# Optimization experiments

Measured on AMD Instinct MI355X. Metric: run time of the kernel, lower is better.

Reference implementation:

```python
import jax, jax.numpy as jnp
import numpy as np

K = 5            # kernel_size per pseudo-dim
N = 51200        # nodes
E = 819200       # edges (avg degree 16)
B = 64           # graphs in batch

# 2^dim corner offsets for degree-1 (linear) open B-spline in dim=2
_BITS = jnp.array([[0, 0], [0, 1], [1, 0], [1, 1]], dtype=jnp.int32)  # [4,2]

def spline_basis(pseudo):
    # pseudo: [E,2] in [0,1]. Returns basis [E,4], weight indices [E,4].
    v = pseudo * (K - 1)
    lo = jnp.clip(jnp.floor(v).astype(jnp.int32), 0, K - 2)   # [E,2]
    frac = v - lo.astype(pseudo.dtype)                        # [E,2]
    idx = lo[:, None, :] + _BITS[None]                        # [E,4,2]
    w = jnp.where(_BITS[None] == 1, frac[:, None, :], 1.0 - frac[:, None, :])
    basis = w.prod(-1)                                        # [E,4]
    widx = idx[..., 0] * K + idx[..., 1]                      # [E,4] in [0,25)
    return basis, widx

def spline_conv(x, src, dst, basis, widx, W, root, bias):
    # x:[N,Fin], W:[25,Fin,Fout], root:[Fin,Fout], bias:[Fout]
    n = x.shape[0]
    Z = jnp.einsum('ni,kio->nko', x, W)          # [N,25,Fout] per-node per-kernel transforms
    Zg = Z[src[:, None], widx]                   # [E,4,Fout] irregular gather
    msg = jnp.einsum('es,eso->eo', basis, Zg)    # [E,Fout]
    agg = jax.ops.segment_sum(msg, dst, num_segments=n)
    deg = jax.ops.segment_sum(jnp.ones_like(msg[:, 0]), dst, num_segments=n)
    agg = agg / jnp.maximum(deg, 1.0)[:, None]   # mean aggregation
    return agg + x @ root + bias

def setup_inputs():
    key = jax.random.key(0)
    ks = jax.random.split(key, 12)
    x = jax.random.normal(ks[0], (N, 7), jnp.float32)
    edge_index = jax.random.randint(ks[1], (2, E), 0, N, dtype=jnp.int32)
    pseudo = jax.random.uniform(ks[2], (E, 2), jnp.float32)
    slices = jnp.arange(B + 1, dtype=jnp.int32) * (N // B)   # graph boundaries
    W1 = jax.random.normal(ks[3], (K * K, 7, 32), jnp.float32) * 0.2
    root1 = jax.random.normal(ks[4], (7, 32), jnp.float32) * 0.2
    b1 = jnp.zeros((32,), jnp.float32)
    W2 = jax.random.normal(ks[5], (K * K, 32, 64), jnp.float32) * 0.1
    root2 = jax.random.normal(ks[6], (32, 64), jnp.float32) * 0.1
    b2 = jnp.zeros((64,), jnp.float32)
    fc_w = jax.random.normal(ks[7], (64, 30), jnp.float32) * 0.1
    fc_b = jnp.zeros((30,), jnp.float32)
    return {"x": x, "edge_index": edge_index, "pseudo": pseudo, "slices": slices,
            "W1": W1, "root1": root1, "b1": b1, "W2": W2, "root2": root2,
            "b2": b2, "fc_w": fc_w, "fc_b": fc_b}

def reference(x, edge_index, pseudo, slices, W1, root1, b1, W2, root2, b2, fc_w, fc_b):
    src, dst = edge_index[0], edge_index[1]
    basis, widx = spline_basis(pseudo)
    h = jax.nn.elu(spline_conv(x, src, dst, basis, widx, W1, root1, b1))
    h = jax.nn.elu(spline_conv(h, src, dst, basis, widx, W2, root2, b2))
    # batch_average: mean of node features per graph (slices = boundaries)
    gid = jnp.clip(jnp.searchsorted(slices, jnp.arange(N), side='right') - 1, 0, B - 1)
    sums = jax.ops.segment_sum(h, gid, num_segments=B)
    counts = (slices[1:] - slices[:-1]).astype(h.dtype)
    g = sums / jnp.maximum(counts, 1.0)[:, None]             # [B,64]
    # dropout is identity in eval mode
    logits = g @ fc_w + fc_b
    return jax.nn.log_softmax(logits, axis=-1)
```

## Files before the change

### kernel.cpp

```cpp
#include <hip/hip_runtime.h>
#include <hip/hip_fp16.h>
#include <math.h>

#define N_NODES 51200
#define N_EDGES 819200
#define NB 64
#define CAP 64

typedef _Float16 half8 __attribute__((ext_vector_type(8)));
typedef __attribute__((ext_vector_type(4))) float float4v;

__device__ __forceinline__ float eluf(float x) {
  return x > 0.f ? x : expm1f(x);
}

__device__ __forceinline__ void dec2(int w0, int w1, int c, float& basf, int& Kc) {
  int K = w0 >> 16;
  float f0 = __half2float(__ushort_as_half((unsigned short)(w1 & 0xFFFF)));
  float f1 = __half2float(__ushort_as_half((unsigned short)(((unsigned)w1) >> 16)));
  float b0 = (c & 2) ? f0 : 1.f - f0;
  float bv = (c & 1) ? f1 : 1.f - f1;
  Kc = K + (c >> 1) * 5 + (c & 1);
  basf = b0 * bv;
}

__device__ __forceinline__ void rmw16(unsigned* Tr, int Kc, int q, float bf, int4 hv) {
  __half2 bas = __float2half2_rn(bf);
  __half2* tp = (__half2*)&Tr[Kc * 16 + q * 4];
  const __half2* h = (const __half2*)&hv;
  __half2 t0 = tp[0], t1 = tp[1], t2 = tp[2], t3 = tp[3];
  tp[0] = __hfma2(bas, h[0], t0);
  tp[1] = __hfma2(bas, h[1], t1);
  tp[2] = __hfma2(bas, h[2], t2);
  tp[3] = __hfma2(bas, h[3], t3);
}

__global__ __launch_bounds__(256) void prep_scatter(
    const float* __restrict__ x, const float* __restrict__ W1,
    const float* __restrict__ root1, const float* __restrict__ W2,
    const float* __restrict__ root2, __half* __restrict__ xh,
    __half* __restrict__ W1T, __half* __restrict__ W2T,
    float* __restrict__ gbuf, const int* __restrict__ ei,
    const float* __restrict__ pseudo, int* __restrict__ cnt,
    int2* __restrict__ bucket) {
  int b = blockIdx.x, tid = threadIdx.x;
  if (b < 400) {
    int base = b * 2048 + tid;
#pragma unroll
    for (int u = 0; u < 8; u++) {
      int e = base + u * 256;
      int src = ei[e], dst = ei[N_EDGES + e];
      float v0 = pseudo[2 * e] * 4.f;
      float v1 = pseudo[2 * e + 1] * 4.f;
      int lo0 = min(max((int)floorf(v0), 0), 3);
      int lo1 = min(max((int)floorf(v1), 0), 3);
      float f0 = v0 - (float)lo0, f1 = v1 - (float)lo1;
      int K = lo0 * 5 + lo1;
      unsigned short u0 = __half_as_ushort(__float2half(f0));
      unsigned short u1 = __half_as_ushort(__float2half(f1));
      int w0 = src | (K << 16);
      int w1 = (int)((unsigned)u0 | ((unsigned)u1 << 16));
      int slot = atomicAdd(&cnt[dst], 1);
      if (slot < CAP) bucket[(size_t)dst * CAP + slot] = make_int2(w0, w1);
    }
    return;
  }
  int bb = b - 400;
  if (bb < 1600) {
    int idx = bb * 256 + tid;
    int n = idx >> 3, j = idx & 7;
    xh[idx] = __float2half((j < 7) ? x[n * 7 + j] : 0.f);
  } else if (bb < 1628) {
    int idx = (bb - 1600) * 256 + tid;
    int o = idx / 224, k = idx - o * 224;
    float v = 0.f;
    if (k < 200) {
      int cell = k >> 3, f = k & 7;
      if (f < 7) v = W1[(cell * 7 + f) * 32 + o];
    } else if (k < 207) {
      v = root1[(k - 200) * 32 + o];
    }
    W1T[idx] = __float2half(v);
  } else if (bb < 1836) {
    int idx = (bb - 1628) * 256 + tid;
    int o = idx / 832, k = idx - o * 832;
    float v = (k < 800) ? W2[k * 64 + o] : root2[(k - 800) * 64 + o];
    W2T[idx] = __float2half(v);
  } else {
    int idx = (bb - 1836) * 256 + tid;
    gbuf[idx] = 0.f;
  }
}

__global__ __launch_bounds__(256) void build_perm(const int* __restrict__ cnt,
                                                  int* __restrict__ perm) {
  __shared__ int hist[65];
  __shared__ int base_s[65];
  int g = blockIdx.x, tid = threadIdx.x;
  int n0 = g * 800;
  if (tid < 65) hist[tid] = 0;
  __syncthreads();
  for (int i = tid; i < 800; i += 256) {
    int d = min(cnt[n0 + i], 64);
    atomicAdd(&hist[d], 1);
  }
  __syncthreads();
  if (tid == 0) {
    int s = 0;
    for (int b = 0; b < 65; b++) { base_s[b] = s; s += hist[b]; }
  }
  __syncthreads();
  for (int i = tid; i < 800; i += 256) {
    int d = min(cnt[n0 + i], 64);
    int pos = atomicAdd(&base_s[d], 1);
    perm[n0 + pos] = n0 + i;
  }
}

#define L1N 16
__global__ __launch_bounds__(256) void fused_l1(const int2* __restrict__ bucket,
                                                const int* __restrict__ cnt,
                                                const int* __restrict__ perm,
                                                const unsigned* __restrict__ xh,
                                                const __half* __restrict__ W1T,
                                                const float* __restrict__ b1,
                                                unsigned short* __restrict__ h1h) {
  __shared__ unsigned T[L1N * 112];
  __shared__ float invdeg_s[L1N];
  __shared__ int pn_s[L1N];
  int tid = threadIdx.x;
  int n0 = blockIdx.x * L1N;
  for (int idx = tid; idx < 448; idx += 256)
    ((int4*)T)[idx] = make_int4(0, 0, 0, 0);
  if (tid < L1N) {
    int pn = perm[n0 + tid];
    pn_s[tid] = pn;
    invdeg_s[tid] = 1.f / fmaxf((float)cnt[pn], 1.f);
  }
  __syncthreads();
  if (tid < L1N * 4) {
    int row = tid >> 2, p = tid & 3;
    int n = pn_s[row];
    float dgc = fmaxf((float)cnt[n], 1.f);
    unsigned xv = xh[n * 4 + p];
    __half2 h = __hmul2(*(const __half2*)&xv, __float2half2_rn(dgc));
    T[row * 112 + 100 + p] = *(unsigned*)&h;
  }
  int wv = tid >> 6, l = tid & 63;
  int slot = l >> 4, c = (l >> 2) & 3, p = l & 3;
  int nn = wv * 4 + slot;
  int n = pn_s[nn];
  int dg = min(cnt[n], CAP);
  int dmax = dg;
  dmax = max(dmax, __shfl_xor(dmax, 16));
  dmax = max(dmax, __shfl_xor(dmax, 32));
  const int2* bk = bucket + (size_t)n * CAP;
  unsigned* Tr = &T[nn * 112];
  int4 ra0 = *(const int4*)(bk + 0);
  int4 rb0 = *(const int4*)(bk + 2);
  int4 ra1 = *(const int4*)(bk + 4);
  int4 rb1 = *(const int4*)(bk + 6);
  unsigned xv0 = xh[(ra0.x & 0xFFFF) * 4 + p];
  unsigned xv1 = xh[(ra0.z & 0xFFFF) * 4 + p];
  unsigned xv2 = xh[(rb0.x & 0xFFFF) * 4 + p];
  unsigned xv3 = xh[(rb0.z & 0xFFFF) * 4 + p];
  for (int j = 0; j < dmax; j += 4) {
    int jp = min(j + 8, CAP - 4);
    int4 ra2 = *(const int4*)(bk + jp);
    int4 rb2 = *(const int4*)(bk + jp + 2);
    unsigned nx0 = xh[(ra1.x & 0xFFFF) * 4 + p];
    unsigned nx1 = xh[(ra1.z & 0xFFFF) * 4 + p];
    unsigned nx2 = xh[(rb1.x & 0xFFFF) * 4 + p];
    unsigned nx3 = xh[(rb1.z & 0xFFFF) * 4 + p];
    bool a0 = j < dg, a1 = j + 1 < dg, a2 = j + 2 < dg, a3 = j + 3 < dg;
    float bf; int Kc;
    if (a0) { dec2(ra0.x, ra0.y, c, bf, Kc);
      __half2* tp = (__half2*)&Tr[Kc * 4 + p];
      *tp = __hfma2(__float2half2_rn(bf), *(const __half2*)&xv0, *tp); }
    if (a1) { dec2(ra0.z, ra0.w, c, bf, Kc);
      __half2* tp = (__half2*)&Tr[Kc * 4 + p];
      *tp = __hfma2(__float2half2_rn(bf), *(const __half2*)&xv1, *tp); }
    if (a2) { dec2(rb0.x, rb0.y, c, bf, Kc);
      __half2* tp = (__half2*)&Tr[Kc * 4 + p];
      *tp = __hfma2(__float2half2_rn(bf), *(const __half2*)&xv2, *tp); }
    if (a3) { dec2(rb0.z, rb0.w, c, bf, Kc);
      __half2* tp = (__half2*)&Tr[Kc * 4 + p];
      *tp = __hfma2(__float2half2_rn(bf), *(const __half2*)&xv3, *tp); }
    ra0 = ra1; rb0 = rb1; ra1 = ra2; rb1 = rb2;
    xv0 = nx0; xv1 = nx1; xv2 = nx2; xv3 = nx3;
  }
  __syncthreads();
  if (wv < 2) {
    int m = l & 15, quad = l >> 4;
    const char* abase = (const char*)T + m * 448 + quad * 16;
    const __half* bbase = W1T + (wv * 16 + m) * 224 + quad * 8;
    float4v acc = {0.f, 0.f, 0.f, 0.f};
#pragma unroll
    for (int it = 0; it < 7; it++) {
      half8 af = *(const half8*)(abase + it * 64);
      half8 bf = *(const half8*)(bbase + it * 32);
      acc = __builtin_amdgcn_mfma_f32_16x16x32_f16(af, bf, acc, 0, 0, 0);
    }
    int feat = wv * 16 + m;
    float bb = b1[feat];
#pragma unroll
    for (int r = 0; r < 4; r++) {
      int row = quad * 4 + r;
      float v = eluf(acc[r] * invdeg_s[row] + bb);
      h1h[(size_t)pn_s[row] * 32 + feat] = __half_as_ushort(__float2half(v));
    }
  }
}

#define L2N 16
__global__ __launch_bounds__(256) void fused_l2(const int2* __restrict__ bucket,
                                                const int* __restrict__ cnt,
                                                const int* __restrict__ perm,
                                                const unsigned* __restrict__ h1hu,
                                                const __half* __restrict__ W2T,
                                                const float* __restrict__ b2,
                                                float* __restrict__ gbuf) {
  __shared__ unsigned T16[L2N * 420];
  __shared__ float invdeg_s[L2N];
  __shared__ int pn_s[L2N];
  int tid = threadIdx.x;
  int n0 = blockIdx.x * L2N;
  for (int idx = tid; idx < 1680; idx += 256)
    ((int4*)T16)[idx] = make_int4(0, 0, 0, 0);
  if (tid < L2N) {
    int pn = perm[n0 + tid];
    pn_s[tid] = pn;
    invdeg_s[tid] = 1.f / fmaxf((float)cnt[pn], 1.f);
  }
  __syncthreads();
  {
    int row = tid >> 4, p = tid & 15;
    int n = pn_s[row];
    float dgc = fmaxf((float)cnt[n], 1.f);
    unsigned hv = h1hu[(size_t)n * 16 + p];
    __half2 h = __hmul2(*(const __half2*)&hv, __float2half2_rn(dgc));
    T16[row * 420 + 400 + p] = *(unsigned*)&h;
  }
  int wv = tid >> 6, l = tid & 63;
  int slot = l >> 4, c = (l >> 2) & 3, q = l & 3;
  int nn = wv * 4 + slot;
  int n = pn_s[nn];
  int dg = min(cnt[n], CAP);
  int dmax = dg;
  dmax = max(dmax, __shfl_xor(dmax, 16));
  dmax = max(dmax, __shfl_xor(dmax, 32));
  const int2* bk = bucket + (size_t)n * CAP;
  unsigned* Tr = &T16[nn * 420];
  const unsigned* h1q = h1hu + q * 4;
  int4 ra0 = *(const int4*)(bk + 0);
  int4 rb0 = *(const int4*)(bk + 2);
  int4 ra1 = *(const int4*)(bk + 4);
  int4 rb1 = *(const int4*)(bk + 6);
  int4 hv0 = *(const int4*)(h1q + (size_t)(ra0.x & 0xFFFF) * 16);
  int4 hv1 = *(const int4*)(h1q + (size_t)(ra0.z & 0xFFFF) * 16);
  int4 hv2 = *(const int4*)(h1q + (size_t)(rb0.x & 0xFFFF) * 16);
  int4 hv3 = *(const int4*)(h1q + (size_t)(rb0.z & 0xFFFF) * 16);
  for (int j = 0; j < dmax; j += 4) {
    int jp = min(j + 8, CAP - 4);
    int4 ra2 = *(const int4*)(bk + jp);
    int4 rb2 = *(const int4*)(bk + jp + 2);
    int4 nh0 = *(const int4*)(h1q + (size_t)(ra1.x & 0xFFFF) * 16);
    int4 nh1 = *(const int4*)(h1q + (size_t)(ra1.z & 0xFFFF) * 16);
    int4 nh2 = *(const int4*)(h1q + (size_t)(rb1.x & 0xFFFF) * 16);
    int4 nh3 = *(const int4*)(h1q + (size_t)(rb1.z & 0xFFFF) * 16);
    bool a0 = j < dg, a1 = j + 1 < dg, a2 = j + 2 < dg, a3 = j + 3 < dg;
    float bf; int Kc;
    if (a0) { dec2(ra0.x, ra0.y, c, bf, Kc); rmw16(Tr, Kc, q, bf, hv0); }
    if (a1) { dec2(ra0.z, ra0.w, c, bf, Kc); rmw16(Tr, Kc, q, bf, hv1); }
    if (a2) { dec2(rb0.x, rb0.y, c, bf, Kc); rmw16(Tr, Kc, q, bf, hv2); }
    if (a3) { dec2(rb0.z, rb0.w, c, bf, Kc); rmw16(Tr, Kc, q, bf, hv3); }
    ra0 = ra1; rb0 = rb1; ra1 = ra2; rb1 = rb2;
    hv0 = nh0; hv1 = nh1; hv2 = nh2; hv3 = nh3;
  }
  __syncthreads();
  int m = l & 15, quad = l >> 4;
  const char* abase = (const char*)T16 + m * 1680 + quad * 16;
  const __half* bbase = W2T + (size_t)(wv * 16 + m) * 832 + quad * 8;
  float4v acc = {0.f, 0.f, 0.f, 0.f};
  half8 bf0 = *(const half8*)(bbase);
  for (int it = 0; it < 26; it++) {
    half8 bfn = *(const half8*)(bbase + min(it + 1, 25) * 32);
    half8 af = *(const half8*)(abase + it * 64);
    acc = __builtin_amdgcn_mfma_f32_16x16x32_f16(af, bf0, acc, 0, 0, 0);
    bf0 = bfn;
  }
  int feat = wv * 16 + m;
  float bb = b2[feat];
  float psum = 0.f;
#pragma unroll
  for (int r = 0; r < 4; r++) {
    int node = quad * 4 + r;
    psum += eluf(acc[r] * invdeg_s[node] + bb);
  }
  psum += __shfl_xor(psum, 16);
  psum += __shfl_xor(psum, 32);
  if (l < 16) {
    int g = n0 / 800;
    atomicAdd(&gbuf[g * 64 + feat], psum);
  }
}

__global__ __launch_bounds__(64) void fc_ls(const float* __restrict__ gbuf,
                                            const int* __restrict__ slices,
                                            const float* __restrict__ fcw,
                                            const float* __restrict__ fcb,
                                            float* __restrict__ out) {
  int g = blockIdx.x;
  int l = threadIdx.x;
  float scale = 1.f / fmaxf((float)(slices[g + 1] - slices[g]), 1.f);
  float logit = -INFINITY;
  if (l < 30) {
    float acc = fcb[l];
    for (int i = 0; i < 64; i++) acc += gbuf[g * 64 + i] * scale * fcw[i * 30 + l];
    logit = acc;
  }
  float m = logit;
  for (int off = 16; off; off >>= 1) m = fmaxf(m, __shfl_xor(m, off, 32));
  float e = (l < 30) ? expf(logit - m) : 0.f;
  for (int off = 16; off; off >>= 1) e += __shfl_xor(e, off, 32);
  if (l < 30) out[g * 30 + l] = logit - m - logf(e);
}

extern "C" void kernel_launch(void* const* d_in, const int* in_sizes, int n_in,
                              void* d_out, int out_size, void* d_ws, size_t ws_size,
                              hipStream_t stream) {
  const float* x      = (const float*)d_in[0];
  const int*   ei     = (const int*)d_in[1];
  const float* pseudo = (const float*)d_in[2];
  const int*   slices = (const int*)d_in[3];
  const float* W1     = (const float*)d_in[4];
  const float* root1  = (const float*)d_in[5];
  const float* b1     = (const float*)d_in[6];
  const float* W2     = (const float*)d_in[7];
  const float* root2  = (const float*)d_in[8];
  const float* b2     = (const float*)d_in[9];
  const float* fcw    = (const float*)d_in[10];
  const float* fcb    = (const float*)d_in[11];
  float* out = (float*)d_out;

  char* ws = (char*)d_ws;
  int*      cnt    = (int*)ws;
  int2*     bucket = (int2*)(cnt + N_NODES);
  unsigned* h1h    = (unsigned*)(bucket + (size_t)N_NODES * CAP);
  float*    gbuf   = (float*)(h1h + (size_t)N_NODES * 16);
  unsigned* xh     = (unsigned*)(gbuf + 64 * 64);
  __half*   W1T    = (__half*)(xh + (size_t)N_NODES * 4);
  __half*   W2T    = W1T + 32 * 224;
  int*      perm   = (int*)(W2T + 64 * 832);

  hipMemsetAsync(cnt, 0, N_NODES * sizeof(int), stream);

  prep_scatter<<<2252, 256, 0, stream>>>(x, W1, root1, W2, root2,
                                         (__half*)xh, W1T, W2T, gbuf,
                                         ei, pseudo, cnt, bucket);
  build_perm<<<NB, 256, 0, stream>>>(cnt, perm);
  fused_l1<<<N_NODES / L1N, 256, 0, stream>>>(bucket, cnt, perm, xh, W1T, b1,
                                              (unsigned short*)h1h);
  fused_l2<<<N_NODES / L2N, 256, 0, stream>>>(bucket, cnt, perm, h1h, W2T, b2,
                                              gbuf);
  fc_ls<<<NB, 64, 0, stream>>>(gbuf, slices, fcw, fcb, out);
}
```

Baseline: 211.5 us.

## Replace fixed-capacity per-node buckets with compact CSR built via count-scan-scatter

The edge records were written into fixed 64-slot buckets per destination node. They are now first stored per edge, then degree counts are prefix-scanned into even-padded offsets across several small kernels, and a second scatter pass writes the records into a compact CSR array. The layer kernels read from that array through a per-node offset. This shrinks the bucket footprint and improves gather locality in the layer kernels, at the cost of three extra launches, an extra pass over the edges and a serial scan.

Result: slower. 252.3 us (+19.3%).

```diff
diff --git a/kernel.cpp b/kernel.cpp
--- a/kernel.cpp
+++ b/kernel.cpp
@@ -35,14 +35,14 @@
   tp[3] = __hfma2(bas, h[3], t3);
 }
 
-__global__ __launch_bounds__(256) void prep_scatter(
+__global__ __launch_bounds__(256) void prep_count(
     const float* __restrict__ x, const float* __restrict__ W1,
     const float* __restrict__ root1, const float* __restrict__ W2,
     const float* __restrict__ root2, __half* __restrict__ xh,
     __half* __restrict__ W1T, __half* __restrict__ W2T,
     float* __restrict__ gbuf, const int* __restrict__ ei,
     const float* __restrict__ pseudo, int* __restrict__ cnt,
-    int2* __restrict__ bucket) {
+    int2* __restrict__ record) {
   int b = blockIdx.x, tid = threadIdx.x;
   if (b < 400) {
     int base = b * 2048 + tid;
@@ -60,8 +60,8 @@
       unsigned short u1 = __half_as_ushort(__float2half(f1));
       int w0 = src | (K << 16);
       int w1 = (int)((unsigned)u0 | ((unsigned)u1 << 16));
-      int slot = atomicAdd(&cnt[dst], 1);
-      if (slot < CAP) bucket[(size_t)dst * CAP + slot] = make_int2(w0, w1);
+      record[e] = make_int2(w0, w1);
+      atomicAdd(&cnt[dst], 1);
     }
     return;
   }
@@ -92,10 +92,13 @@
   }
 }
 
-__global__ __launch_bounds__(256) void build_perm(const int* __restrict__ cnt,
-                                                  int* __restrict__ perm) {
+__global__ __launch_bounds__(256) void build_perm2(const int* __restrict__ cnt,
+                                                   int* __restrict__ perm,
+                                                   int* __restrict__ offl,
+                                                   int* __restrict__ wsum) {
   __shared__ int hist[65];
   __shared__ int base_s[65];
+  __shared__ int tsum[256];
   int g = blockIdx.x, tid = threadIdx.x;
   int n0 = g * 800;
   if (tid < 65) hist[tid] = 0;
@@ -115,12 +118,70 @@
     int pos = atomicAdd(&base_s[d], 1);
     perm[n0 + pos] = n0 + i;
   }
+  int loc[4], s = 0;
+#pragma unroll
+  for (int i = 0; i < 4; i++) {
+    int idx = tid * 4 + i;
+    int pd = 0;
+    if (idx < 800) { int d = cnt[n0 + idx]; pd = (d + 1) & ~1; }
+    loc[i] = s; s += pd;
+  }
+  tsum[tid] = s;
+  __syncthreads();
+  if (tid == 0) {
+    int acc = 0;
+    for (int t = 0; t < 256; t++) { int v = tsum[t]; tsum[t] = acc; acc += v; }
+    wsum[g] = acc;
+  }
+  __syncthreads();
+  int b0 = tsum[tid];
+#pragma unroll
+  for (int i = 0; i < 4; i++) {
+    int idx = tid * 4 + i;
+    if (idx < 800) offl[n0 + idx] = b0 + loc[i];
+  }
+}
+
+__global__ __launch_bounds__(64) void wscan(const int* __restrict__ wsum,
+                                            int* __restrict__ wbase) {
+  if (threadIdx.x == 0) {
+    int acc = 0;
+    for (int g = 0; g < NB; g++) { wbase[g] = acc; acc += wsum[g]; }
+  }
+}
+
+__global__ __launch_bounds__(256) void fin_off(const int* __restrict__ offl,
+                                               const int* __restrict__ wbase,
+                                               int* __restrict__ offv,
+                                               int* __restrict__ wc) {
+  int n = blockIdx.x * 256 + threadIdx.x;
+  if (n < N_NODES) {
+    int o = offl[n] + wbase[n / 800];
+    offv[n] = o;
+    wc[n] = o;
+  }
+}
+
+__global__ __launch_bounds__(256) void scatter2(const int* __restrict__ ei,
+                                                const int2* __restrict__ record,
+                                                int* __restrict__ wc,
+                                                int2* __restrict__ bucket) {
+  int base = blockIdx.x * 2048 + threadIdx.x;
+#pragma unroll
+  for (int u = 0; u < 8; u++) {
+    int e = base + u * 256;
+    int dst = ei[N_EDGES + e];
+    int2 r = record[e];
+    int slot = atomicAdd(&wc[dst], 1);
+    bucket[slot] = r;
+  }
 }
 
 #define L1N 16
 __global__ __launch_bounds__(256) void fused_l1(const int2* __restrict__ bucket,
                                                 const int* __restrict__ cnt,
                                                 const int* __restrict__ perm,
+                                                const int* __restrict__ offv,
                                                 const unsigned* __restrict__ xh,
                                                 const __half* __restrict__ W1T,
                                                 const float* __restrict__ b1,
@@ -128,6 +189,7 @@
   __shared__ unsigned T[L1N * 112];
   __shared__ float invdeg_s[L1N];
   __shared__ int pn_s[L1N];
+  __shared__ int off_s[L1N];
   int tid = threadIdx.x;
   int n0 = blockIdx.x * L1N;
   for (int idx = tid; idx < 448; idx += 256)
@@ -135,6 +197,7 @@
   if (tid < L1N) {
     int pn = perm[n0 + tid];
     pn_s[tid] = pn;
+    off_s[tid] = offv[pn];
     invdeg_s[tid] = 1.f / fmaxf((float)cnt[pn], 1.f);
   }
   __syncthreads();
@@ -154,7 +217,7 @@
   int dmax = dg;
   dmax = max(dmax, __shfl_xor(dmax, 16));
   dmax = max(dmax, __shfl_xor(dmax, 32));
-  const int2* bk = bucket + (size_t)n * CAP;
+  const int2* bk = bucket + off_s[nn];
   unsigned* Tr = &T[nn * 112];
   int4 ra0 = *(const int4*)(bk + 0);
   int4 rb0 = *(const int4*)(bk + 2);
@@ -216,6 +279,7 @@
 __global__ __launch_bounds__(256) void fused_l2(const int2* __restrict__ bucket,
                                                 const int* __restrict__ cnt,
                                                 const int* __restrict__ perm,
+                                                const int* __restrict__ offv,
                                                 const unsigned* __restrict__ h1hu,
                                                 const __half* __restrict__ W2T,
                                                 const float* __restrict__ b2,
@@ -223,6 +287,7 @@
   __shared__ unsigned T16[L2N * 420];
   __shared__ float invdeg_s[L2N];
   __shared__ int pn_s[L2N];
+  __shared__ int off_s[L2N];
   int tid = threadIdx.x;
   int n0 = blockIdx.x * L2N;
   for (int idx = tid; idx < 1680; idx += 256)
@@ -230,6 +295,7 @@
   if (tid < L2N) {
     int pn = perm[n0 + tid];
     pn_s[tid] = pn;
+    off_s[tid] = offv[pn];
     invdeg_s[tid] = 1.f / fmaxf((float)cnt[pn], 1.f);
   }
   __syncthreads();
@@ -249,7 +315,7 @@
   int dmax = dg;
   dmax = max(dmax, __shfl_xor(dmax, 16));
   dmax = max(dmax, __shfl_xor(dmax, 32));
-  const int2* bk = bucket + (size_t)n * CAP;
+  const int2* bk = bucket + off_s[nn];
   unsigned* Tr = &T16[nn * 420];
   const unsigned* h1q = h1hu + q * 4;
   int4 ra0 = *(const int4*)(bk + 0);
@@ -345,23 +411,32 @@
 
   char* ws = (char*)d_ws;
   int*      cnt    = (int*)ws;
-  int2*     bucket = (int2*)(cnt + N_NODES);
-  unsigned* h1h    = (unsigned*)(bucket + (size_t)N_NODES * CAP);
+  int2*     record = (int2*)(cnt + N_NODES);
+  int2*     bucket = record + N_EDGES;
+  unsigned* h1h    = (unsigned*)(bucket + N_EDGES + N_NODES + 64);
   float*    gbuf   = (float*)(h1h + (size_t)N_NODES * 16);
   unsigned* xh     = (unsigned*)(gbuf + 64 * 64);
   __half*   W1T    = (__half*)(xh + (size_t)N_NODES * 4);
   __half*   W2T    = W1T + 32 * 224;
   int*      perm   = (int*)(W2T + 64 * 832);
+  int*      offl   = perm + N_NODES;
+  int*      offv   = offl + N_NODES;
+  int*      wc     = offv + N_NODES;
+  int*      wsumv  = wc + N_NODES;
+  int*      wbasev = wsumv + NB;
 
   hipMemsetAsync(cnt, 0, N_NODES * sizeof(int), stream);
 
-  prep_scatter<<<2252, 256, 0, stream>>>(x, W1, root1, W2, root2,
-                                         (__half*)xh, W1T, W2T, gbuf,
-                                         ei, pseudo, cnt, bucket);
-  build_perm<<<NB, 256, 0, stream>>>(cnt, perm);
-  fused_l1<<<N_NODES / L1N, 256, 0, stream>>>(bucket, cnt, perm, xh, W1T, b1,
-                                              (unsigned short*)h1h);
-  fused_l2<<<N_NODES / L2N, 256, 0, stream>>>(bucket, cnt, perm, h1h, W2T, b2,
-                                              gbuf);
+  prep_count<<<2252, 256, 0, stream>>>(x, W1, root1, W2, root2,
+                                       (__half*)xh, W1T, W2T, gbuf,
+                                       ei, pseudo, cnt, record);
+  build_perm2<<<NB, 256, 0, stream>>>(cnt, perm, offl, wsumv);
+  wscan<<<1, 64, 0, stream>>>(wsumv, wbasev);
+  fin_off<<<200, 256, 0, stream>>>(offl, wbasev, offv, wc);
+  scatter2<<<400, 256, 0, stream>>>(ei, record, wc, bucket);
+  fused_l1<<<N_NODES / L1N, 256, 0, stream>>>(bucket, cnt, perm, offv, xh,
+                                              W1T, b1, (unsigned short*)h1h);
+  fused_l2<<<N_NODES / L2N, 256, 0, stream>>>(bucket, cnt, perm, offv, h1h,
+                                              W2T, b2, gbuf);
   fc_ls<<<NB, 64, 0, stream>>>(gbuf, slices, fcw, fcb, out);
 }
```
